# Kernel optimization log

Hardware: AMD Instinct MI355X
Metric: run time of the kernel (lower is better)

The kernel has to match this reference:

```python
import jax, jax.numpy as jnp
from jax import lax
import numpy as np

K_LIST = [2, 4, 8]

def setup_inputs() -> dict:
    key = jax.random.key(0)
    k1, k2 = jax.random.split(key)
    B_, C, H, Wd = 8, 256, 128, 128
    x = jax.random.normal(k1, (B_, C, H, Wd), dtype=jnp.float32)
    # conv weights init ~ N(0, 1e-6) per the module's 'zero' init, bias zero
    W = jax.random.normal(k2, (len(K_LIST), 1, C, 3, 3), dtype=jnp.float32) * 1e-6
    Bb = jnp.zeros((len(K_LIST), 1), dtype=jnp.float32)
    return {"x": x, "W": W, "B": Bb}


def _band_grid(h, w):
    # signed max of (fftfreq_h, rfftfreq_w) coords, matching torch code
    fh = jnp.fft.fftfreq(h).astype(jnp.float32)          # [h]
    fw = jnp.fft.rfftfreq(w).astype(jnp.float32)         # [w//2+1]
    return jnp.maximum(fh[:, None], fw[None, :])         # [h, w//2+1]


def reference(x, W, B):
    b, c, h, w = x.shape
    x_dtype = x.dtype
    x32 = x.astype(jnp.float32)
    x_fft = jnp.fft.rfft2(x32, norm='ortho')             # [b,c,h,w//2+1] complex
    grid = _band_grid(h, w)
    pre_x = x32
    out = jnp.zeros_like(x32)
    for idx, freq in enumerate(K_LIST):
        mask = (grid < 0.5 / freq).astype(jnp.float32)   # [h, w//2+1]
        low = jnp.fft.irfft2(x_fft * mask, s=(h, w), norm='ortho')
        high = pre_x - low
        pre_x = low
        # Conv2d(in=256, out=1, k=3, pad=1) on att_feat=x
        fwgt = lax.conv_general_dilated(
            x32, W[idx], window_strides=(1, 1), padding='SAME',
            dimension_numbers=('NCHW', 'OIHW', 'NCHW'))
        fwgt = fwgt + B[idx][None, :, None, None]        # [b,1,h,w]
        gate = jax.nn.sigmoid(fwgt) * 2.0
        out = out + gate * high                          # broadcast over channels
    out = out + pre_x                                    # residual low-frequency part
    return out.astype(x_dtype)
```

## Files before the change

### kernel.cpp

```cpp
#include <hip/hip_runtime.h>


#define NPIX 16384
#define NCHN 256

typedef __attribute__((ext_vector_type(8))) short bf16x8;
typedef __attribute__((ext_vector_type(4))) float f32x4;

__device__ __align__(16) short g_f[64][128];
__device__ __align__(16) short g_h[192][256];
__device__ __align__(16) short g_e[3][256][192];
__device__ __align__(16) short g_p[3][128][64];

static __device__ __forceinline__ short f2bf(float f) {
  unsigned u = __float_as_uint(f);
  unsigned r = (u + 0x7fffu + ((u >> 16) & 1u)) >> 16;
  return (short)r;
}
static __device__ __forceinline__ float bf2f(short s) {
  return __uint_as_float(((unsigned)(unsigned short)s) << 16);
}
static __device__ __forceinline__ f32x4 mfma16(bf16x8 a, bf16x8 b, f32x4 c) {
  return __builtin_amdgcn_mfma_f32_16x16x32_bf16(a, b, c, 0, 0, 0);
}

static __device__ void const_fill(int idx) {
  const float C = 6.2831853071795864769f / 128.f;
  if (idx < 8192) {
    int n = idx >> 7, q = idx & 127;
    int j = n & 31;
    float ang = C * (float)((j * q) & 127);
    float v = (n < 32) ? cosf(ang) : -sinf(ang);
    reinterpret_cast<short*>(g_f)[idx] = f2bf(v);
  } else if (idx < 57344) {
    int e = idx - 8192;
    int d = e >> 8, kk = e & 255;
    int r = (d < 96) ? d : d - 96;
    int ifr = (r < 32) ? r : r + 32;
    float ang = C * (float)((ifr * (kk & 127)) & 127);
    float cv = cosf(ang) * (1.f / 128.f), sv = sinf(ang) * (1.f / 128.f);
    float v = (d < 96) ? ((kk < 128) ? cv : sv) : ((kk < 128) ? -sv : cv);
    reinterpret_cast<short*>(g_h)[e] = f2bf(v);
  } else if (idx < 204800) {
    int e = idx - 57344;
    int k = e / 49152; int e2 = e % 49152;
    int mm = e2 / 192, kk = e2 % 192;
    int nk = 32 >> k;
    int r = (kk < 96) ? kk : kk - 96;
    bool allow = (r < nk) || (r >= 32);
    int ifr = (r < 32) ? r : r + 32;
    float ang = C * (float)((ifr * (mm & 127)) & 127);
    float cv = cosf(ang), sv = sinf(ang);
    float v = (mm < 128) ? ((kk < 96) ? cv : -sv) : ((kk < 96) ? sv : cv);
    reinterpret_cast<short*>(g_e)[e] = f2bf(allow ? v : 0.f);
  } else if (idx < 229376) {
    int e = idx - 204800;
    int k = e / 8192; int e2 = e % 8192;
    int n = e2 >> 6, jj = e2 & 63;
    int nk = 32 >> k;
    int j = jj & 31;
    bool valid = (j < nk) && (jj < 32 || j > 0);
    float wj = (j == 0) ? (1.f / 128.f) : (2.f / 128.f);
    float ang = C * (float)((j * n) & 127);
    float v = (jj < 32) ? (wj * cosf(ang)) : (-wj * sinf(ang));
    reinterpret_cast<short*>(g_p)[e] = f2bf(valid ? v : 0.f);
  }
}

__global__ __launch_bounds__(256) void gates_partial_kernel(
    const float* __restrict__ x, const float* __restrict__ Wg,
    float* __restrict__ partial) {
  int bid = blockIdx.x;
  if (bid >= 2048) {
    const_fill((bid - 2048) * 256 + threadIdx.x);
    return;
  }
  int b = bid & 7;
  int tile = (bid >> 3) & 63;
  int cs = bid >> 9;
  int m = ((tile >> 3) << 4) + (threadIdx.x >> 4);
  int n = ((tile & 7) << 4) + (threadIdx.x & 15);
  float a0 = 0.f, a1 = 0.f, a2 = 0.f;
  const float* xb = x + (size_t)b * NCHN * NPIX;
  for (int c = cs * 64; c < cs * 64 + 64; ++c) {
    const float* xc = xb + (size_t)c * NPIX;
    const float* wc = Wg + c * 9;
    #pragma unroll
    for (int dh = -1; dh <= 1; ++dh) {
      int gm = m + dh;
      bool vm = (unsigned)gm < 128u;
      #pragma unroll
      for (int dw = -1; dw <= 1; ++dw) {
        int gn = n + dw;
        float xv = (vm && (unsigned)gn < 128u) ? xc[gm * 128 + gn] : 0.f;
        int tap = (dh + 1) * 3 + (dw + 1);
        a0 = fmaf(xv, wc[tap], a0);
        a1 = fmaf(xv, wc[2304 + tap], a1);
        a2 = fmaf(xv, wc[4608 + tap], a2);
      }
    }
  }
  int pix = m * 128 + n;
  float* pp = partial + (size_t)(cs * 8 + b) * 3 * NPIX;
  pp[pix]            = a0;
  pp[NPIX + pix]     = a1;
  pp[2 * NPIX + pix] = a2;
}

__global__ __launch_bounds__(256) void gates_combine_kernel(
    const float* __restrict__ partial, const float* __restrict__ Bg,
    short* __restrict__ dcoef) {
  int bid = blockIdx.x;
  int b = bid & 7;
  int px = (bid >> 3) * 256 + threadIdx.x;
  float a0 = Bg[0], a1 = Bg[1], a2 = Bg[2];
  #pragma unroll
  for (int cs = 0; cs < 4; ++cs) {
    const float* pp = partial + (size_t)(cs * 8 + b) * 3 * NPIX;
    a0 += pp[px];
    a1 += pp[NPIX + px];
    a2 += pp[2 * NPIX + px];
  }
  float g1 = 2.f / (1.f + expf(-a0));
  float g2 = 2.f / (1.f + expf(-a1));
  float g3 = 2.f / (1.f + expf(-a2));
  int pix = b * NPIX + px;
  dcoef[pix]          = f2bf(g1 - 1.f);
  dcoef[131072 + pix] = f2bf(g2 - g1);
  dcoef[262144 + pix] = f2bf(g3 - g2);
  dcoef[393216 + pix] = f2bf(1.f - g3);
}

__global__ __launch_bounds__(256) void gates_kernel(
    const float* __restrict__ x, const float* __restrict__ Wg,
    const float* __restrict__ Bg, short* __restrict__ dcoef) {
  int blk = blockIdx.x;
  if (blk >= 512) {
    const_fill((blk - 512) * 256 + threadIdx.x);
    return;
  }
  int b = blk >> 6;
  int tile = blk & 63;
  int m = ((tile >> 3) << 4) + (threadIdx.x >> 4);
  int n = ((tile & 7) << 4) + (threadIdx.x & 15);
  float a0 = 0.f, a1 = 0.f, a2 = 0.f;
  const float* xb = x + (size_t)b * NCHN * NPIX;
  for (int c = 0; c < NCHN; ++c) {
    const float* xc = xb + (size_t)c * NPIX;
    const float* wc = Wg + c * 9;
    #pragma unroll
    for (int dh = -1; dh <= 1; ++dh) {
      int gm = m + dh;
      bool vm = (unsigned)gm < 128u;
      #pragma unroll
      for (int dw = -1; dw <= 1; ++dw) {
        int gn = n + dw;
        float xv = (vm && (unsigned)gn < 128u) ? xc[gm * 128 + gn] : 0.f;
        int tap = (dh + 1) * 3 + (dw + 1);
        a0 = fmaf(xv, wc[tap], a0);
        a1 = fmaf(xv, wc[2304 + tap], a1);
        a2 = fmaf(xv, wc[4608 + tap], a2);
      }
    }
  }
  a0 += Bg[0]; a1 += Bg[1]; a2 += Bg[2];
  float g1 = 2.f / (1.f + expf(-a0));
  float g2 = 2.f / (1.f + expf(-a1));
  float g3 = 2.f / (1.f + expf(-a2));
  int pix = b * NPIX + m * 128 + n;
  dcoef[pix]          = f2bf(g1 - 1.f);
  dcoef[131072 + pix] = f2bf(g2 - g1);
  dcoef[262144 + pix] = f2bf(g3 - g2);
  dcoef[393216 + pix] = f2bf(1.f - g3);
}

__global__ __launch_bounds__(512, 2) void fbm_kernel(
    const float* __restrict__ x, const short* __restrict__ dcoef,
    float* __restrict__ out) {
  __shared__ __align__(16) short Xs[16384];
  __shared__ __align__(16) short WVs[8192];
  __shared__ __align__(16) short Ds2[6144];
  char* XsB = reinterpret_cast<char*>(Xs);
  char* PlaneB = XsB;
  char* WsB = reinterpret_cast<char*>(WVs);
  char* DsB = reinterpret_cast<char*>(Ds2);

  int t = threadIdx.x;
  int bid = blockIdx.x;
  int b = bid >> 5;
  int cg = bid & 31;
  size_t img0 = ((size_t)b << 8) + ((size_t)cg << 3);
  int lane = t & 63, w = t >> 6;
  int l15 = lane & 15, l4 = lane >> 4;
  const f32x4 zero = {0.f, 0.f, 0.f, 0.f};

  const short4* d0p = reinterpret_cast<const short4*>(dcoef + ((size_t)b << 14));

  for (int c = 0; c < 8; ++c) {
    f32x4 oaccC[8];
    {
      const f32x4* xv4 = reinterpret_cast<const f32x4*>(x + (img0 + c) * NPIX);
      #pragma unroll
      for (int i = 0; i < 8; ++i) {
        int f = t + i * 512;
        f32x4 xv = __builtin_nontemporal_load(&xv4[f]);
        short4 dv = d0p[f];
        f32x4 dvf = {bf2f(dv.x), bf2f(dv.y), bf2f(dv.z), bf2f(dv.w)};
        oaccC[i] = xv + dvf * xv;
        int row = f >> 5;
        int byte = row * 256 + (((f & 31) * 8) ^ ((row & 7) << 4));
        short4 s;
        s.x = f2bf(xv[0]); s.y = f2bf(xv[1]); s.z = f2bf(xv[2]); s.w = f2bf(xv[3]);
        *reinterpret_cast<short4*>(XsB + byte) = s;
      }
    }
    __syncthreads();

    {
      int Ntile = w & 3, Mq = w >> 2;
      int n = Ntile * 16 + l15;
      f32x4 acc[4] = {zero, zero, zero, zero};
      #pragma unroll
      for (int ks = 0; ks < 4; ++ks) {
        int koff = ks * 32 + l4 * 8;
        bf16x8 bf = *reinterpret_cast<const bf16x8*>(&g_f[n][koff]);
        #pragma unroll
        for (int mt = 0; mt < 4; ++mt) {
          int p = (Mq * 4 + mt) * 16 + l15;
          bf16x8 a = *reinterpret_cast<const bf16x8*>(
              XsB + p * 256 + ((koff * 2) ^ ((p & 7) << 4)));
          acc[mt] = mfma16(a, bf, acc[mt]);
        }
      }
      #pragma unroll
      for (int mt = 0; mt < 4; ++mt) {
        int p0 = (Mq * 4 + mt) * 16 + l4 * 4;
        short4 s;
        s.x = f2bf(acc[mt][0]); s.y = f2bf(acc[mt][1]);
        s.z = f2bf(acc[mt][2]); s.w = f2bf(acc[mt][3]);
        *reinterpret_cast<short4*>(WsB + n * 256 + ((p0 * 2) ^ ((n & 7) << 4))) = s;
      }
    }
    __syncthreads();

    {
      int Ntile = w & 1, Mt3 = w >> 1;
      int n = Ntile * 16 + l15;
      f32x4 acc[3] = {zero, zero, zero};
      #pragma unroll
      for (int ks = 0; ks < 8; ++ks) {
        int koff = ks * 32 + l4 * 8;
        int wrow = n + ((ks >= 4) ? 32 : 0);
        bf16x8 bb = *reinterpret_cast<const bf16x8*>(
            WsB + wrow * 256 + (((koff & 127) * 2) ^ ((wrow & 7) << 4)));
        #pragma unroll
        for (int mt = 0; mt < 3; ++mt) {
          int d = (Mt3 * 3 + mt) * 16 + l15;
          bf16x8 aa = *reinterpret_cast<const bf16x8*>(&g_h[d][koff]);
          acc[mt] = mfma16(aa, bb, acc[mt]);
        }
      }
      #pragma unroll
      for (int mt = 0; mt < 3; ++mt) {
        int d0 = (Mt3 * 3 + mt) * 16 + l4 * 4;
        short4 s;
        s.x = f2bf(acc[mt][0]); s.y = f2bf(acc[mt][1]);
        s.z = f2bf(acc[mt][2]); s.w = f2bf(acc[mt][3]);
        *reinterpret_cast<short4*>(DsB + n * 384 + ((d0 * 2) ^ ((n & 7) << 4))) = s;
      }
    }
    __syncthreads();

    int Mg3 = w >> 2, Ng3 = w & 3;
    for (int k = 0; k < 3; ++k) {
      {
        f32x4 acc[2][2] = {{zero, zero}, {zero, zero}};
        #pragma unroll
        for (int ks = 0; ks < 6; ++ks) {
          int koff = ks * 32 + l4 * 8;
          bf16x8 b0 = *reinterpret_cast<const bf16x8*>(
              DsB + l15 * 384 + ((koff * 2) ^ ((l15 & 7) << 4)));
          int j1 = 16 + l15;
          bf16x8 b1 = *reinterpret_cast<const bf16x8*>(
              DsB + j1 * 384 + ((koff * 2) ^ ((j1 & 7) << 4)));
          #pragma unroll
          for (int mi = 0; mi < 2; ++mi) {
            int mstk = (2 * w + mi) * 16 + l15;
            bf16x8 aa = *reinterpret_cast<const bf16x8*>(&g_e[k][mstk][koff]);
            acc[mi][0] = mfma16(aa, b0, acc[mi][0]);
            acc[mi][1] = mfma16(aa, b1, acc[mi][1]);
          }
        }
        #pragma unroll
        for (int mi = 0; mi < 2; ++mi) {
          #pragma unroll
          for (int ni = 0; ni < 2; ++ni) {
            int j = ni * 16 + l15;
            #pragma unroll
            for (int r = 0; r < 4; ++r) {
              int mstk = (2 * w + mi) * 16 + l4 * 4 + r;
              int m = mstk & 127;
              int jst = ((mstk >> 7) << 5) + j;
              *reinterpret_cast<short*>(WsB + m * 128 + ((jst * 2) ^ ((m & 7) << 4))) =
                  f2bf(acc[mi][ni][r]);
            }
          }
        }
      }
      __syncthreads();
      {
        f32x4 acc[4][2] = {{zero, zero}, {zero, zero}, {zero, zero}, {zero, zero}};
        #pragma unroll
        for (int ks = 0; ks < 2; ++ks) {
          int koff = ks * 32 + l4 * 8;
          bf16x8 bfr[2];
          #pragma unroll
          for (int nt = 0; nt < 2; ++nt) {
            int nout = (Ng3 * 2 + nt) * 16 + l15;
            bfr[nt] = *reinterpret_cast<const bf16x8*>(&g_p[k][nout][koff]);
          }
          #pragma unroll
          for (int mt = 0; mt < 4; ++mt) {
            int m = (Mg3 * 4 + mt) * 16 + l15;
            bf16x8 aa = *reinterpret_cast<const bf16x8*>(
                WsB + m * 128 + ((koff * 2) ^ ((m & 7) << 4)));
            acc[mt][0] = mfma16(aa, bfr[0], acc[mt][0]);
            acc[mt][1] = mfma16(aa, bfr[1], acc[mt][1]);
          }
        }
        #pragma unroll
        for (int mt = 0; mt < 4; ++mt) {
          #pragma unroll
          for (int nt = 0; nt < 2; ++nt) {
            int col = (Ng3 * 2 + nt) * 16 + l15;
            #pragma unroll
            for (int r = 0; r < 4; ++r) {
              int row = (Mg3 * 4 + mt) * 16 + l4 * 4 + r;
              int byte = row * 256 + ((col ^ ((row & 7) << 2)) << 1);
              *reinterpret_cast<short*>(PlaneB + byte) = f2bf(acc[mt][nt][r]);
            }
          }
        }
      }
      __syncthreads();
      {
        const short4* dk = reinterpret_cast<const short4*>(
            dcoef + (size_t)(k + 1) * 131072 + ((size_t)b << 14));
        #pragma unroll
        for (int i = 0; i < 8; ++i) {
          int f = t + i * 512;
          int row = f >> 5;
          int col = (f & 31) * 4;
          int byte = row * 256 + ((col ^ ((row & 7) << 2)) << 1);
          short4 s = *reinterpret_cast<const short4*>(PlaneB + byte);
          short4 dv = dk[f];
          oaccC[i][0] = fmaf(bf2f(dv.x), bf2f(s.x), oaccC[i][0]);
          oaccC[i][1] = fmaf(bf2f(dv.y), bf2f(s.y), oaccC[i][1]);
          oaccC[i][2] = fmaf(bf2f(dv.z), bf2f(s.z), oaccC[i][2]);
          oaccC[i][3] = fmaf(bf2f(dv.w), bf2f(s.w), oaccC[i][3]);
        }
      }
      __syncthreads();
    }

    f32x4* og4 = reinterpret_cast<f32x4*>(out + (img0 + c) * NPIX);
    #pragma unroll
    for (int i = 0; i < 8; ++i) og4[t + i * 512] = oaccC[i];
  }
}

extern "C" void kernel_launch(void* const* d_in, const int* in_sizes, int n_in,
                              void* d_out, int out_size, void* d_ws, size_t ws_size,
                              hipStream_t stream) {
  const float* x  = (const float*)d_in[0];
  const float* Wg = (const float*)d_in[1];
  const float* Bg = (const float*)d_in[2];
  float* out  = (float*)d_out;
  short* dcoef = (short*)d_ws;
  float* partial = (float*)((char*)d_ws + (1u << 20));
  if (ws_size >= (size_t)(8u << 20)) {
    gates_partial_kernel<<<2944, 256, 0, stream>>>(x, Wg, partial);
    gates_combine_kernel<<<512, 256, 0, stream>>>(partial, Bg, dcoef);
  } else {
    gates_kernel<<<1408, 256, 0, stream>>>(x, Wg, Bg, dcoef);
  }
  fbm_kernel<<<256, 512, 0, stream>>>(x, dcoef, out);
}
```

Baseline: 303.6 us.

## Cut register pressure in fbm kernel to double occupancy and grid size

Raises launch bounds from 2 to 4 blocks per CU and doubles the grid to 512 blocks, each handling 4 channels instead of 8. To fit the register budget, the fp32 output accumulators become packed bf16 accumulators, x is reloaded at the end for the residual term, and the MFMA loops are split so fewer accumulator tiles are live at once. LDS use is about 60 KB per block, so four resident blocks may exceed the CU's LDS capacity and cap the real occupancy gain. The bf16 accumulation of band contributions lowers precision, and re-reading x adds global traffic.

```diff
diff --git a/kernel.cpp b/kernel.cpp
--- a/kernel.cpp
+++ b/kernel.cpp
@@ -174,7 +174,7 @@
   dcoef[393216 + pix] = f2bf(1.f - g3);
 }
 
-__global__ __launch_bounds__(512, 2) void fbm_kernel(
+__global__ __launch_bounds__(512, 4) void fbm_kernel(
     const float* __restrict__ x, const short* __restrict__ dcoef,
     float* __restrict__ out) {
   __shared__ __align__(16) short Xs[16384];
@@ -187,26 +187,26 @@
 
   int t = threadIdx.x;
   int bid = blockIdx.x;
-  int b = bid >> 5;
-  int cg = bid & 31;
-  size_t img0 = ((size_t)b << 8) + ((size_t)cg << 3);
+  int b = bid >> 6;
+  int cg = bid & 63;
+  size_t img0 = ((size_t)b << 8) + ((size_t)cg << 2);
   int lane = t & 63, w = t >> 6;
   int l15 = lane & 15, l4 = lane >> 4;
   const f32x4 zero = {0.f, 0.f, 0.f, 0.f};
 
   const short4* d0p = reinterpret_cast<const short4*>(dcoef + ((size_t)b << 14));
 
-  for (int c = 0; c < 8; ++c) {
-    f32x4 oaccC[8];
+  for (int c = 0; c < 4; ++c) {
+    unsigned dacc[16];
+    #pragma unroll
+    for (int i = 0; i < 16; ++i) dacc[i] = 0u;
+
     {
       const f32x4* xv4 = reinterpret_cast<const f32x4*>(x + (img0 + c) * NPIX);
       #pragma unroll
       for (int i = 0; i < 8; ++i) {
         int f = t + i * 512;
-        f32x4 xv = __builtin_nontemporal_load(&xv4[f]);
-        short4 dv = d0p[f];
-        f32x4 dvf = {bf2f(dv.x), bf2f(dv.y), bf2f(dv.z), bf2f(dv.w)};
-        oaccC[i] = xv + dvf * xv;
+        f32x4 xv = xv4[f];
         int row = f >> 5;
         int byte = row * 256 + (((f & 31) * 8) ^ ((row & 7) << 4));
         short4 s;
@@ -219,26 +219,29 @@
     {
       int Ntile = w & 3, Mq = w >> 2;
       int n = Ntile * 16 + l15;
-      f32x4 acc[4] = {zero, zero, zero, zero};
-      #pragma unroll
-      for (int ks = 0; ks < 4; ++ks) {
-        int koff = ks * 32 + l4 * 8;
-        bf16x8 bf = *reinterpret_cast<const bf16x8*>(&g_f[n][koff]);
-        #pragma unroll
-        for (int mt = 0; mt < 4; ++mt) {
-          int p = (Mq * 4 + mt) * 16 + l15;
-          bf16x8 a = *reinterpret_cast<const bf16x8*>(
-              XsB + p * 256 + ((koff * 2) ^ ((p & 7) << 4)));
-          acc[mt] = mfma16(a, bf, acc[mt]);
-        }
-      }
-      #pragma unroll
-      for (int mt = 0; mt < 4; ++mt) {
-        int p0 = (Mq * 4 + mt) * 16 + l4 * 4;
-        short4 s;
-        s.x = f2bf(acc[mt][0]); s.y = f2bf(acc[mt][1]);
-        s.z = f2bf(acc[mt][2]); s.w = f2bf(acc[mt][3]);
-        *reinterpret_cast<short4*>(WsB + n * 256 + ((p0 * 2) ^ ((n & 7) << 4))) = s;
+      #pragma unroll
+      for (int h = 0; h < 2; ++h) {
+        f32x4 acc[2] = {zero, zero};
+        #pragma unroll
+        for (int ks = 0; ks < 4; ++ks) {
+          int koff = ks * 32 + l4 * 8;
+          bf16x8 bf = *reinterpret_cast<const bf16x8*>(&g_f[n][koff]);
+          #pragma unroll
+          for (int mt = 0; mt < 2; ++mt) {
+            int p = (Mq * 4 + h * 2 + mt) * 16 + l15;
+            bf16x8 a = *reinterpret_cast<const bf16x8*>(
+                XsB + p * 256 + ((koff * 2) ^ ((p & 7) << 4)));
+            acc[mt] = mfma16(a, bf, acc[mt]);
+          }
+        }
+        #pragma unroll
+        for (int mt = 0; mt < 2; ++mt) {
+          int p0 = (Mq * 4 + h * 2 + mt) * 16 + l4 * 4;
+          short4 s;
+          s.x = f2bf(acc[mt][0]); s.y = f2bf(acc[mt][1]);
+          s.z = f2bf(acc[mt][2]); s.w = f2bf(acc[mt][3]);
+          *reinterpret_cast<short4*>(WsB + n * 256 + ((p0 * 2) ^ ((n & 7) << 4))) = s;
+        }
       }
     }
     __syncthreads();
@@ -246,26 +249,23 @@
     {
       int Ntile = w & 1, Mt3 = w >> 1;
       int n = Ntile * 16 + l15;
-      f32x4 acc[3] = {zero, zero, zero};
-      #pragma unroll
-      for (int ks = 0; ks < 8; ++ks) {
-        int koff = ks * 32 + l4 * 8;
-        int wrow = n + ((ks >= 4) ? 32 : 0);
-        bf16x8 bb = *reinterpret_cast<const bf16x8*>(
-            WsB + wrow * 256 + (((koff & 127) * 2) ^ ((wrow & 7) << 4)));
-        #pragma unroll
-        for (int mt = 0; mt < 3; ++mt) {
+      #pragma unroll
+      for (int mt = 0; mt < 3; ++mt) {
+        f32x4 acc = zero;
+        #pragma unroll
+        for (int ks = 0; ks < 8; ++ks) {
+          int koff = ks * 32 + l4 * 8;
+          int wrow = n + ((ks >= 4) ? 32 : 0);
+          bf16x8 bb = *reinterpret_cast<const bf16x8*>(
+              WsB + wrow * 256 + (((koff & 127) * 2) ^ ((wrow & 7) << 4)));
           int d = (Mt3 * 3 + mt) * 16 + l15;
           bf16x8 aa = *reinterpret_cast<const bf16x8*>(&g_h[d][koff]);
-          acc[mt] = mfma16(aa, bb, acc[mt]);
-        }
-      }
-      #pragma unroll
-      for (int mt = 0; mt < 3; ++mt) {
+          acc = mfma16(aa, bb, acc);
+        }
         int d0 = (Mt3 * 3 + mt) * 16 + l4 * 4;
         short4 s;
-        s.x = f2bf(acc[mt][0]); s.y = f2bf(acc[mt][1]);
-        s.z = f2bf(acc[mt][2]); s.w = f2bf(acc[mt][3]);
+        s.x = f2bf(acc[0]); s.y = f2bf(acc[1]);
+        s.z = f2bf(acc[2]); s.w = f2bf(acc[3]);
         *reinterpret_cast<short4*>(DsB + n * 384 + ((d0 * 2) ^ ((n & 7) << 4))) = s;
       }
     }
@@ -273,72 +273,58 @@
 
     int Mg3 = w >> 2, Ng3 = w & 3;
     for (int k = 0; k < 3; ++k) {
-      {
-        f32x4 acc[2][2] = {{zero, zero}, {zero, zero}};
+      #pragma unroll
+      for (int ni = 0; ni < 2; ++ni) {
+        f32x4 acc[2] = {zero, zero};
+        int jn = ni * 16 + l15;
         #pragma unroll
         for (int ks = 0; ks < 6; ++ks) {
           int koff = ks * 32 + l4 * 8;
-          bf16x8 b0 = *reinterpret_cast<const bf16x8*>(
-              DsB + l15 * 384 + ((koff * 2) ^ ((l15 & 7) << 4)));
-          int j1 = 16 + l15;
-          bf16x8 b1 = *reinterpret_cast<const bf16x8*>(
-              DsB + j1 * 384 + ((koff * 2) ^ ((j1 & 7) << 4)));
+          bf16x8 bn = *reinterpret_cast<const bf16x8*>(
+              DsB + jn * 384 + ((koff * 2) ^ ((jn & 7) << 4)));
           #pragma unroll
           for (int mi = 0; mi < 2; ++mi) {
             int mstk = (2 * w + mi) * 16 + l15;
             bf16x8 aa = *reinterpret_cast<const bf16x8*>(&g_e[k][mstk][koff]);
-            acc[mi][0] = mfma16(aa, b0, acc[mi][0]);
-            acc[mi][1] = mfma16(aa, b1, acc[mi][1]);
+            acc[mi] = mfma16(aa, bn, acc[mi]);
           }
         }
         #pragma unroll
         for (int mi = 0; mi < 2; ++mi) {
           #pragma unroll
-          for (int ni = 0; ni < 2; ++ni) {
-            int j = ni * 16 + l15;
-            #pragma unroll
-            for (int r = 0; r < 4; ++r) {
-              int mstk = (2 * w + mi) * 16 + l4 * 4 + r;
-              int m = mstk & 127;
-              int jst = ((mstk >> 7) << 5) + j;
-              *reinterpret_cast<short*>(WsB + m * 128 + ((jst * 2) ^ ((m & 7) << 4))) =
-                  f2bf(acc[mi][ni][r]);
-            }
+          for (int r = 0; r < 4; ++r) {
+            int mstk = (2 * w + mi) * 16 + l4 * 4 + r;
+            int m = mstk & 127;
+            int jst = ((mstk >> 7) << 5) + jn;
+            *reinterpret_cast<short*>(WsB + m * 128 + ((jst * 2) ^ ((m & 7) << 4))) =
+                f2bf(acc[mi][r]);
           }
         }
       }
       __syncthreads();
-      {
-        f32x4 acc[4][2] = {{zero, zero}, {zero, zero}, {zero, zero}, {zero, zero}};
+      #pragma unroll
+      for (int nt = 0; nt < 2; ++nt) {
+        f32x4 acc[4] = {zero, zero, zero, zero};
+        int nout = (Ng3 * 2 + nt) * 16 + l15;
         #pragma unroll
         for (int ks = 0; ks < 2; ++ks) {
           int koff = ks * 32 + l4 * 8;
-          bf16x8 bfr[2];
-          #pragma unroll
-          for (int nt = 0; nt < 2; ++nt) {
-            int nout = (Ng3 * 2 + nt) * 16 + l15;
-            bfr[nt] = *reinterpret_cast<const bf16x8*>(&g_p[k][nout][koff]);
-          }
+          bf16x8 bfr = *reinterpret_cast<const bf16x8*>(&g_p[k][nout][koff]);
           #pragma unroll
           for (int mt = 0; mt < 4; ++mt) {
             int m = (Mg3 * 4 + mt) * 16 + l15;
             bf16x8 aa = *reinterpret_cast<const bf16x8*>(
                 WsB + m * 128 + ((koff * 2) ^ ((m & 7) << 4)));
-            acc[mt][0] = mfma16(aa, bfr[0], acc[mt][0]);
-            acc[mt][1] = mfma16(aa, bfr[1], acc[mt][1]);
+            acc[mt] = mfma16(aa, bfr, acc[mt]);
           }
         }
         #pragma unroll
         for (int mt = 0; mt < 4; ++mt) {
           #pragma unroll
-          for (int nt = 0; nt < 2; ++nt) {
-            int col = (Ng3 * 2 + nt) * 16 + l15;
-            #pragma unroll
-            for (int r = 0; r < 4; ++r) {
-              int row = (Mg3 * 4 + mt) * 16 + l4 * 4 + r;
-              int byte = row * 256 + ((col ^ ((row & 7) << 2)) << 1);
-              *reinterpret_cast<short*>(PlaneB + byte) = f2bf(acc[mt][nt][r]);
-            }
+          for (int r = 0; r < 4; ++r) {
+            int row = (Mg3 * 4 + mt) * 16 + l4 * 4 + r;
+            int byte = row * 256 + ((nout ^ ((row & 7) << 2)) << 1);
+            *reinterpret_cast<short*>(PlaneB + byte) = f2bf(acc[mt][r]);
           }
         }
       }
@@ -354,18 +340,37 @@
           int byte = row * 256 + ((col ^ ((row & 7) << 2)) << 1);
           short4 s = *reinterpret_cast<const short4*>(PlaneB + byte);
           short4 dv = dk[f];
-          oaccC[i][0] = fmaf(bf2f(dv.x), bf2f(s.x), oaccC[i][0]);
-          oaccC[i][1] = fmaf(bf2f(dv.y), bf2f(s.y), oaccC[i][1]);
-          oaccC[i][2] = fmaf(bf2f(dv.z), bf2f(s.z), oaccC[i][2]);
-          oaccC[i][3] = fmaf(bf2f(dv.w), bf2f(s.w), oaccC[i][3]);
+          unsigned a0 = dacc[2 * i], a1 = dacc[2 * i + 1];
+          float l0 = fmaf(bf2f(dv.x), bf2f(s.x), bf2f((short)(a0 & 0xffff)));
+          float l1 = fmaf(bf2f(dv.y), bf2f(s.y), bf2f((short)(a0 >> 16)));
+          float l2 = fmaf(bf2f(dv.z), bf2f(s.z), bf2f((short)(a1 & 0xffff)));
+          float l3 = fmaf(bf2f(dv.w), bf2f(s.w), bf2f((short)(a1 >> 16)));
+          dacc[2 * i] = (unsigned)(unsigned short)f2bf(l0) |
+                        ((unsigned)(unsigned short)f2bf(l1) << 16);
+          dacc[2 * i + 1] = (unsigned)(unsigned short)f2bf(l2) |
+                            ((unsigned)(unsigned short)f2bf(l3) << 16);
         }
       }
       __syncthreads();
     }
 
-    f32x4* og4 = reinterpret_cast<f32x4*>(out + (img0 + c) * NPIX);
-    #pragma unroll
-    for (int i = 0; i < 8; ++i) og4[t + i * 512] = oaccC[i];
+    {
+      const f32x4* xv4 = reinterpret_cast<const f32x4*>(x + (img0 + c) * NPIX);
+      f32x4* og4 = reinterpret_cast<f32x4*>(out + (img0 + c) * NPIX);
+      #pragma unroll
+      for (int i = 0; i < 8; ++i) {
+        int f = t + i * 512;
+        f32x4 xv = xv4[f];
+        short4 dv = d0p[f];
+        unsigned a0 = dacc[2 * i], a1 = dacc[2 * i + 1];
+        f32x4 o;
+        o[0] = fmaf(bf2f(dv.x), xv[0], xv[0]) + bf2f((short)(a0 & 0xffff));
+        o[1] = fmaf(bf2f(dv.y), xv[1], xv[1]) + bf2f((short)(a0 >> 16));
+        o[2] = fmaf(bf2f(dv.z), xv[2], xv[2]) + bf2f((short)(a1 & 0xffff));
+        o[3] = fmaf(bf2f(dv.w), xv[3], xv[3]) + bf2f((short)(a1 >> 16));
+        __builtin_nontemporal_store(o, &og4[f]);
+      }
+    }
   }
 }
 
@@ -384,5 +389,5 @@
   } else {
     gates_kernel<<<1408, 256, 0, stream>>>(x, Wg, Bg, dcoef);
   }
-  fbm_kernel<<<256, 512, 0, stream>>>(x, dcoef, out);
-}
+  fbm_kernel<<<512, 512, 0, stream>>>(x, dcoef, out);
+}
```

Result: slower. 387.5 us (+27.6%).
